# Optimization experiments

Measured on AMD Instinct MI355X. Metric: run time of the kernel, lower is better.

Reference implementation:

```python
import jax, jax.numpy as jnp
import numpy as np

N_PAPER, N_MESH = 60000, 30000
N = N_PAPER + N_MESH
E_TRAIN, E_DEC = 2000000, 400000
F_PAPER = F_MESH = 128
D0, H, D = 16, 32, 16  # initial embed, hidden, final embed
NREL, NB = 2, 4


def _glorot(key, shape):
    fan_in, fan_out = shape[-2], shape[-1]
    s = jnp.sqrt(6.0 / (fan_in + fan_out)).astype(jnp.float32)
    return jax.random.uniform(key, shape, jnp.float32, -s, s)


def setup_inputs() -> dict:
    key = jax.random.key(0)
    ks = iter(jax.random.split(key, 40))
    inp = {
        'x_paper': jax.random.normal(next(ks), (N_PAPER, F_PAPER), jnp.float32),
        'x_mesh': jax.random.normal(next(ks), (N_MESH, F_MESH), jnp.float32),
        'train_edge_index': jax.random.randint(next(ks), (2, E_TRAIN), 0, N, jnp.int64 if jax.config.jax_enable_x64 else jnp.int32),
        'train_edge_type': jnp.sort(jax.random.randint(next(ks), (E_TRAIN,), 0, NREL)),
        'pos_edge_index': jax.random.randint(next(ks), (2, E_DEC), 0, N),
        'pos_edge_type': jnp.sort(jax.random.randint(next(ks), (E_DEC,), 0, NREL)),
        'neg_edge_index': jax.random.randint(next(ks), (2, E_DEC), 0, N),
        'neg_edge_type': jnp.sort(jax.random.randint(next(ks), (E_DEC,), 0, NREL)),
        # input transforms
        'Wp': _glorot(next(ks), (F_PAPER, D0)), 'bp': jnp.zeros((D0,), jnp.float32),
        'Wm': _glorot(next(ks), (F_MESH, D0)), 'bm': jnp.zeros((D0,), jnp.float32),
        # decode linears
        'Wd0': _glorot(next(ks), (D, D)), 'bd0': jnp.zeros((D,), jnp.float32),
        'Wd1': _glorot(next(ks), (D, D)), 'bd1': jnp.zeros((D,), jnp.float32),
    }
    dims = [(D0, H), (H, H), (H, H), (H, D)]
    for i, (di, do) in enumerate(dims, 1):
        inp[f'bases{i}'] = _glorot(next(ks), (NB, di, do))
        inp[f'comp{i}'] = _glorot(next(ks), (NREL, NB))
        inp[f'root{i}'] = _glorot(next(ks), (di, do))
        inp[f'bias{i}'] = jnp.zeros((do,), jnp.float32)
    return inp


def rgcn_layer(x, src, dst, et, bases, comp, root, bias):
    # PyG RGCNConv with basis decomposition, per-relation mean aggregation.
    out = x @ root + bias
    xs = x[src]  # [E, in]
    for r in range(NREL):
        W_r = jnp.einsum('b,bio->io', comp[r], bases)
        m = xs @ W_r  # [E, out]
        mf = (et == r).astype(m.dtype)
        cnt = jax.ops.segment_sum(mf, dst, num_segments=N)
        agg = jax.ops.segment_sum(m * mf[:, None], dst, num_segments=N)
        out = out + agg / jnp.clip(cnt, 1.0)[:, None]
    return out


def _decode_block(z, ei, et, Wd0, bd0, Wd1, bd1):
    zs, zd = z[ei[0]], z[ei[1]]
    h0 = zs @ Wd0 + bd0
    h1 = zs @ Wd1 + bd1
    h = jnp.where((et == 0)[:, None], h0, h1)
    return jnp.sum(h * zd, axis=-1)


def reference(x_paper, x_mesh, train_edge_index, train_edge_type,
              pos_edge_index, pos_edge_type, neg_edge_index, neg_edge_type,
              Wp, bp, Wm, bm, Wd0, bd0, Wd1, bd1,
              bases1, comp1, root1, bias1, bases2, comp2, root2, bias2,
              bases3, comp3, root3, bias3, bases4, comp4, root4, bias4):
    x = jnp.concatenate([x_paper @ Wp + bp, x_mesh @ Wm + bm], axis=0)  # [N, D0]
    src, dst = train_edge_index[0], train_edge_index[1]
    x = jax.nn.relu(rgcn_layer(x, src, dst, train_edge_type, bases1, comp1, root1, bias1))
    x = jax.nn.relu(rgcn_layer(x, src, dst, train_edge_type, bases2, comp2, root2, bias2))
    x = jax.nn.relu(rgcn_layer(x, src, dst, train_edge_type, bases3, comp3, root3, bias3))
    z = rgcn_layer(x, src, dst, train_edge_type, bases4, comp4, root4, bias4)
    # edge types are sorted, so per-edge in-order compute matches the masked concat order
    pos = _decode_block(z, pos_edge_index, pos_edge_type, Wd0, bd0, Wd1, bd1)
    neg = _decode_block(z, neg_edge_index, neg_edge_type, Wd0, bd0, Wd1, bd1)
    return jnp.concatenate([pos, neg], axis=0)  # [2*E_DEC]
```

## Files before the change

kernel.cpp:

```cpp
#include <hip/hip_runtime.h>
#include <hip/hip_bf16.h>

constexpr int NN = 90000;
constexpr int NP = 60000;
constexpr int NM = 30000;
constexpr int ET = 2000000;
constexpr int ED = 400000;
constexpr int TWO_NN = 2 * NN;

constexpr int BKT_SH  = 10;
constexpr int NB_BKT  = (TWO_NN + 1023) >> BKT_SH;
constexpr int BKT_CAP = 12288;
constexpr int TILE    = 2048;
constexpr int N_TILES = (ET + TILE - 1) / TILE;

__device__ __forceinline__ float bflo(unsigned int u) {
    union { unsigned int i; float f; } c;
    c.i = u << 16;
    return c.f;
}
__device__ __forceinline__ float bfhi(unsigned int u) {
    union { unsigned int i; float f; } c;
    c.i = u & 0xffff0000u;
    return c.f;
}
__device__ __forceinline__ unsigned short f2bf(float f) {
    union { float f; unsigned int i; } c;
    c.f = f;
    unsigned int x = c.i;
    return (unsigned short)((x + 0x7FFFu + ((x >> 16) & 1u)) >> 16);
}

__global__ void init_kernel(const int* __restrict__ tei, int* __restrict__ gcur,
                            int* __restrict__ dflag) {
    int b = blockIdx.x * blockDim.x + threadIdx.x;
    if (b < NB_BKT) gcur[b] = b * BKT_CAP;
    if (b == 0) {
        int allzero = 1;
        for (int i = 0; i < 16; i++)
            if (tei[2 * i + 1] != 0) allzero = 0;
        dflag[0] = allzero;
    }
}

__global__ void __launch_bounds__(256) binA_kernel(
        const int* __restrict__ ei, const int* __restrict__ et,
        const int* __restrict__ dflag, int* __restrict__ gcur,
        int2* __restrict__ pairs) {
    __shared__ int hist[NB_BKT];
    __shared__ int excl[NB_BKT];
    __shared__ int cur[NB_BKT];
    __shared__ int gbase[NB_BKT];
    __shared__ int scn[256];
    __shared__ int2 tbuf[TILE];
    int t = threadIdx.x;
    int tile0 = blockIdx.x * TILE;
    int tcount = ET - tile0;
    if (tcount > TILE) tcount = TILE;
    for (int i = t; i < NB_BKT; i += 256) hist[i] = 0;
    __syncthreads();
    int sft = dflag[0];
    int myk[8], mys[8];
#pragma unroll
    for (int q = 0; q < 8; q++) {
        int li = q * 256 + t;
        myk[q] = -1;
        if (li < tcount) {
            int e = tile0 + li;
            int s = ei[(size_t)e << sft];
            int d = ei[(size_t)(ET + e) << sft];
            int r = et[(size_t)e << sft];
            int key = r * NN + d;
            myk[q] = key;
            mys[q] = s;
            atomicAdd(&hist[key >> BKT_SH], 1);
        }
    }
    __syncthreads();
    int v = (t < NB_BKT) ? hist[t] : 0;
    scn[t] = v;
    __syncthreads();
    for (int st = 1; st < 256; st <<= 1) {
        int u = (t >= st) ? scn[t - st] : 0;
        __syncthreads();
        scn[t] += u;
        __syncthreads();
    }
    if (t < NB_BKT) {
        excl[t] = scn[t] - v;
        cur[t] = scn[t] - v;
    }
    __syncthreads();
#pragma unroll
    for (int q = 0; q < 8; q++) {
        if (myk[q] >= 0) {
            int b = myk[q] >> BKT_SH;
            int p = atomicAdd(&cur[b], 1);
            tbuf[p] = make_int2(myk[q], mys[q]);
        }
    }
    __syncthreads();
    if (t < NB_BKT && hist[t] > 0) gbase[t] = atomicAdd(&gcur[t], hist[t]);
    __syncthreads();
    for (int i = t; i < tcount; i += 256) {
        int2 p = tbuf[i];
        int b = p.x >> BKT_SH;
        int gpos = gbase[b] + (i - excl[b]);
        int cap = (b + 1) * BKT_CAP - 1;
        pairs[gpos < cap ? gpos : cap] = p;
    }
}

__global__ void __launch_bounds__(256) histB_kernel(
        const int* __restrict__ gcur, const int2* __restrict__ pairs,
        int* __restrict__ off, int* __restrict__ endo, float* __restrict__ inv) {
    __shared__ int kh[1024];
    __shared__ int scn[256];
    int b = blockIdx.x;
    int t = threadIdx.x;
    for (int i = t; i < 1024; i += 256) kh[i] = 0;
    __syncthreads();
    int beg = b * BKT_CAP, end = gcur[b];
    for (int i = beg + t; i < end; i += 256)
        atomicAdd(&kh[pairs[i].x & 1023], 1);
    __syncthreads();
    int v[4];
    int s = 0;
#pragma unroll
    for (int q = 0; q < 4; q++) {
        v[q] = kh[t * 4 + q];
        s += v[q];
    }
    scn[t] = s;
    __syncthreads();
    for (int st = 1; st < 256; st <<= 1) {
        int u = (t >= st) ? scn[t - st] : 0;
        __syncthreads();
        scn[t] += u;
        __syncthreads();
    }
    int run = b * BKT_CAP + scn[t] - s;
    int kbase = b << BKT_SH;
#pragma unroll
    for (int q = 0; q < 4; q++) {
        int key = kbase + t * 4 + q;
        if (key < TWO_NN) {
            off[key] = run;
            endo[key] = run + v[q];
            inv[key] = 1.0f / (float)(v[q] > 1 ? v[q] : 1);
        }
        run += v[q];
    }
}

__global__ void __launch_bounds__(256) placeB_kernel(
        const int* __restrict__ gcur, const int2* __restrict__ pairs,
        const int* __restrict__ off, int* __restrict__ csr) {
    __shared__ int kc[1024];
    int b = blockIdx.x;
    int t = threadIdx.x;
    int kbase = b << BKT_SH;
    for (int i = t; i < 1024; i += 256)
        if (kbase + i < TWO_NN) kc[i] = off[kbase + i];
    __syncthreads();
    int beg = b * BKT_CAP, end = gcur[b];
    for (int i = beg + t; i < end; i += 256) {
        int2 p = pairs[i];
        int pos = atomicAdd(&kc[p.x & 1023], 1);
        csr[pos] = p.y;
    }
}

__global__ void __launch_bounds__(256) embed2_kernel(
        const float* __restrict__ Xp, const float* __restrict__ Xm,
        const float* __restrict__ Wp, const float* __restrict__ bp,
        const float* __restrict__ Wm, const float* __restrict__ bm,
        float* __restrict__ out, unsigned short* __restrict__ outbf) {
    __shared__ float Wl[4096 + 32];
    for (int i = threadIdx.x; i < 2048; i += 256) {
        Wl[i] = Wp[i];
        Wl[2048 + i] = Wm[i];
    }
    if (threadIdx.x < 16) {
        Wl[4096 + threadIdx.x] = bp[threadIdx.x];
        Wl[4112 + threadIdx.x] = bm[threadIdx.x];
    }
    __syncthreads();
    int n = blockIdx.x * 256 + threadIdx.x;
    if (n >= NN) return;
    const float* X;
    const float* Ws;
    const float* Bs;
    if (n < NP) { X = Xp + (size_t)n * 128; Ws = Wl; Bs = Wl + 4096; }
    else        { X = Xm + (size_t)(n - NP) * 128; Ws = Wl + 2048; Bs = Wl + 4112; }
    float acc[16];
#pragma unroll
    for (int j = 0; j < 16; j++) acc[j] = Bs[j];
    const float4* row = (const float4*)X;
    for (int k4 = 0; k4 < 32; k4++) {
        float4 xv = row[k4];
        int k = k4 * 4;
#pragma unroll
        for (int j = 0; j < 16; j++) {
            float a = acc[j];
            a = fmaf(xv.x, Ws[(k + 0) * 16 + j], a);
            a = fmaf(xv.y, Ws[(k + 1) * 16 + j], a);
            a = fmaf(xv.z, Ws[(k + 2) * 16 + j], a);
            a = fmaf(xv.w, Ws[(k + 3) * 16 + j], a);
            acc[j] = a;
        }
    }
    float4* o = (float4*)(out + (size_t)n * 16);
    ushort4* ob = (ushort4*)(outbf + (size_t)n * 16);
#pragma unroll
    for (int q = 0; q < 4; q++) {
        o[q] = make_float4(acc[4 * q], acc[4 * q + 1], acc[4 * q + 2], acc[4 * q + 3]);
        ushort4 ub;
        ub.x = f2bf(acc[4 * q]);     ub.y = f2bf(acc[4 * q + 1]);
        ub.z = f2bf(acc[4 * q + 2]); ub.w = f2bf(acc[4 * q + 3]);
        ob[q] = ub;
    }
}

__global__ void prep_all_kernel(
        const float* __restrict__ ba0, const float* __restrict__ co0,
        const float* __restrict__ ro0, const float* __restrict__ bi0,
        const float* __restrict__ ba1, const float* __restrict__ co1,
        const float* __restrict__ ro1, const float* __restrict__ bi1,
        const float* __restrict__ ba2, const float* __restrict__ co2,
        const float* __restrict__ ro2, const float* __restrict__ bi2,
        const float* __restrict__ ba3, const float* __restrict__ co3,
        const float* __restrict__ ro3, const float* __restrict__ bi3,
        float* __restrict__ Wbuf4) {
    int l = blockIdx.x;
    const float* bases; const float* comp; const float* root; const float* bias;
    if (l == 0)      { bases = ba0; comp = co0; root = ro0; bias = bi0; }
    else if (l == 1) { bases = ba1; comp = co1; root = ro1; bias = bi1; }
    else if (l == 2) { bases = ba2; comp = co2; root = ro2; bias = bi2; }
    else             { bases = ba3; comp = co3; root = ro3; bias = bi3; }
    int din = (l == 0) ? 16 : 32;
    int dout = (l == 3) ? 16 : 32;
    int sz = din * dout;
    float* W = Wbuf4 + l * 3200;
    for (int i = threadIdx.x; i < sz; i += 256) {
        float b0 = bases[i];
        float b1 = bases[sz + i];
        float b2 = bases[2 * sz + i];
        float b3 = bases[3 * sz + i];
        for (int r = 0; r < 2; r++) {
            W[r * sz + i] = comp[r * 4 + 0] * b0 + comp[r * 4 + 1] * b1 +
                            comp[r * 4 + 2] * b2 + comp[r * 4 + 3] * b3;
        }
        W[2 * sz + i] = root[i];
    }
    if (threadIdx.x < dout) W[3 * sz + threadIdx.x] = bias[threadIdx.x];
}

template <int DIN, int DOUT, int RELU, int WBF>
__global__ void __launch_bounds__(256) layer_kernel(
        const int* __restrict__ off, const int* __restrict__ endo,
        const int* __restrict__ csr,
        const float* __restrict__ xin, const unsigned short* __restrict__ xbf_in,
        const float* __restrict__ inv, const float* __restrict__ Wbuf,
        float* __restrict__ xout, unsigned short* __restrict__ xbf_out) {
    constexpr int SZ = DIN * DOUT;
    constexpr int QL = DIN / 8;
    constexpr int TPN = 2 * QL;
    constexpr int NPB = 256 / TPN;
    constexpr int AGST = 2 * DIN + 4;
    constexpr int XSST = DIN + 4;
    __shared__ float Wl[3 * SZ + DOUT];
    __shared__ float agg[NPB * AGST];
    __shared__ float xs[NPB * XSST];
    for (int i = threadIdx.x; i < 3 * SZ + DOUT; i += 256) Wl[i] = Wbuf[i];
    int t = threadIdx.x;
    int ln = t / TPN;
    int rl = t % TPN;
    int r = rl / QL;
    int lane = rl % QL;
    int d = blockIdx.x * NPB + ln;
    if (d < NN) {
        *(float4*)(xs + ln * XSST + rl * 4) =
            *(const float4*)(xin + (size_t)d * DIN + rl * 4);
        int key = r * NN + d;
        int b = off[key];
        int e = endo[key];
        float a0[8] = {0, 0, 0, 0, 0, 0, 0, 0};
        float a1[8] = {0, 0, 0, 0, 0, 0, 0, 0};
        const unsigned short* hp = xbf_in + lane * 8;
        int k = b;
        for (; k + 1 < e; k += 2) {
            int s0 = csr[k];
            int s1 = csr[k + 1];
            uint4 u0 = *(const uint4*)(hp + (size_t)s0 * DIN);
            uint4 u1 = *(const uint4*)(hp + (size_t)s1 * DIN);
            a0[0] += bflo(u0.x); a0[1] += bfhi(u0.x);
            a0[2] += bflo(u0.y); a0[3] += bfhi(u0.y);
            a0[4] += bflo(u0.z); a0[5] += bfhi(u0.z);
            a0[6] += bflo(u0.w); a0[7] += bfhi(u0.w);
            a1[0] += bflo(u1.x); a1[1] += bfhi(u1.x);
            a1[2] += bflo(u1.y); a1[3] += bfhi(u1.y);
            a1[4] += bflo(u1.z); a1[5] += bfhi(u1.z);
            a1[6] += bflo(u1.w); a1[7] += bfhi(u1.w);
        }
        if (k < e) {
            uint4 u0 = *(const uint4*)(hp + (size_t)csr[k] * DIN);
            a0[0] += bflo(u0.x); a0[1] += bfhi(u0.x);
            a0[2] += bflo(u0.y); a0[3] += bfhi(u0.y);
            a0[4] += bflo(u0.z); a0[5] += bfhi(u0.z);
            a0[6] += bflo(u0.w); a0[7] += bfhi(u0.w);
        }
        float* ap = agg + ln * AGST + r * DIN + lane * 8;
        *(float4*)ap = make_float4(a0[0] + a1[0], a0[1] + a1[1],
                                   a0[2] + a1[2], a0[3] + a1[3]);
        *(float4*)(ap + 4) = make_float4(a0[4] + a1[4], a0[5] + a1[5],
                                         a0[6] + a1[6], a0[7] + a1[7]);
    }
    __syncthreads();
    constexpr int CPN = DOUT / 4;
    for (int tt = t; tt < NPB * CPN; tt += 256) {
        int ln2 = tt / CPN;
        int j0 = (tt % CPN) * 4;
        int d2 = blockIdx.x * NPB + ln2;
        if (d2 < NN) {
            float iv0 = inv[d2], iv1 = inv[NN + d2];
            float acc[4];
#pragma unroll
            for (int jj = 0; jj < 4; jj++) acc[jj] = Wl[3 * SZ + j0 + jj];
#pragma unroll
            for (int k = 0; k < DIN; k++) {
                float xv = xs[ln2 * XSST + k];
                float m0 = agg[ln2 * AGST + k] * iv0;
                float m1 = agg[ln2 * AGST + DIN + k] * iv1;
                const float* w0 = &Wl[k * DOUT + j0];
                const float* w1 = &Wl[SZ + k * DOUT + j0];
                const float* wr = &Wl[2 * SZ + k * DOUT + j0];
#pragma unroll
                for (int jj = 0; jj < 4; jj++) {
                    acc[jj] = fmaf(xv, wr[jj], acc[jj]);
                    acc[jj] = fmaf(m0, w0[jj], acc[jj]);
                    acc[jj] = fmaf(m1, w1[jj], acc[jj]);
                }
            }
            if (RELU) {
#pragma unroll
                for (int jj = 0; jj < 4; jj++) acc[jj] = fmaxf(acc[jj], 0.0f);
            }
            *(float4*)(xout + (size_t)d2 * DOUT + j0) =
                make_float4(acc[0], acc[1], acc[2], acc[3]);
            if (WBF) {
                ushort4 ub;
                ub.x = f2bf(acc[0]); ub.y = f2bf(acc[1]);
                ub.z = f2bf(acc[2]); ub.w = f2bf(acc[3]);
                *(ushort4*)(xbf_out + (size_t)d2 * DOUT + j0) = ub;
            }
        }
    }
}

__global__ void __launch_bounds__(256) decode_fused_kernel(
        const float* __restrict__ z,
        const float* __restrict__ Wd0, const float* __restrict__ bd0,
        const float* __restrict__ Wd1, const float* __restrict__ bd1,
        const int* __restrict__ pei, const int* __restrict__ pet,
        const int* __restrict__ nei, const int* __restrict__ net_,
        float* __restrict__ out, const int* __restrict__ dflag) {
    __shared__ float W[2][256];
    __shared__ float B[2][16];
    for (int i = threadIdx.x; i < 256; i += 256) {
        W[0][i] = Wd0[i];
        W[1][i] = Wd1[i];
    }
    if (threadIdx.x < 16) {
        B[0][threadIdx.x] = bd0[threadIdx.x];
        B[1][threadIdx.x] = bd1[threadIdx.x];
    }
    __syncthreads();
    int i = blockIdx.x * 256 + threadIdx.x;
    if (i >= 2 * ED) return;
    int sft = dflag[0];
    const int* ei;
    const int* et;
    int e;
    if (i < ED) { ei = pei; et = pet; e = i; }
    else        { ei = nei; et = net_; e = i - ED; }
    int s = ei[(size_t)e << sft];
    int d = ei[(size_t)(ED + e) << sft];
    int r = et[(size_t)e << sft];
    float zs[16], zd[16];
    const float4* sp = (const float4*)(z + ((size_t)s << 4));
    const float4* dp = (const float4*)(z + ((size_t)d << 4));
#pragma unroll
    for (int q = 0; q < 4; q++) {
        float4 a = sp[q];
        float4 b = dp[q];
        zs[4 * q] = a.x; zs[4 * q + 1] = a.y; zs[4 * q + 2] = a.z; zs[4 * q + 3] = a.w;
        zd[4 * q] = b.x; zd[4 * q + 1] = b.y; zd[4 * q + 2] = b.z; zd[4 * q + 3] = b.w;
    }
    const float* Wr = W[r];
    const float* Br = B[r];
    float acc = 0.0f;
#pragma unroll
    for (int j = 0; j < 16; j++) {
        float yj = Br[j];
#pragma unroll
        for (int k = 0; k < 16; k++) yj = fmaf(zs[k], Wr[k * 16 + j], yj);
        acc = fmaf(yj, zd[j], acc);
    }
    out[i] = acc;
}

extern "C" void kernel_launch(void* const* d_in, const int* in_sizes, int n_in,
                              void* d_out, int out_size, void* d_ws, size_t ws_size,
                              hipStream_t stream) {
    const float* x_paper = (const float*)d_in[0];
    const float* x_mesh  = (const float*)d_in[1];
    const int* tei  = (const int*)d_in[2];
    const int* tet  = (const int*)d_in[3];
    const int* pei  = (const int*)d_in[4];
    const int* pet  = (const int*)d_in[5];
    const int* nei  = (const int*)d_in[6];
    const int* net_ = (const int*)d_in[7];
    const float* Wp  = (const float*)d_in[8];
    const float* bp  = (const float*)d_in[9];
    const float* Wm  = (const float*)d_in[10];
    const float* bm  = (const float*)d_in[11];
    const float* Wd0 = (const float*)d_in[12];
    const float* bd0 = (const float*)d_in[13];
    const float* Wd1 = (const float*)d_in[14];
    const float* bd1 = (const float*)d_in[15];

    float* ws = (float*)d_ws;
    size_t o = 0;
    float* bufA = ws + o; o += (size_t)NN * 32;
    float* bufB = ws + o; o += (size_t)NN * 32;
    unsigned short* xbfA = (unsigned short*)(ws + o); o += (size_t)NN * 16;
    unsigned short* xbfB = (unsigned short*)(ws + o); o += (size_t)NN * 16;
    float* inv  = ws + o; o += (size_t)TWO_NN;
    int*   off  = (int*)(ws + o); o += (size_t)TWO_NN;
    int*   endo = (int*)(ws + o); o += (size_t)TWO_NN;
    int*   csr  = (int*)(ws + o); o += (size_t)NB_BKT * BKT_CAP;
    int*   gcur = (int*)(ws + o); o += 256;
    int2*  pairs = (int2*)(ws + o); o += (size_t)2 * NB_BKT * BKT_CAP;
    float* Wbuf4 = ws + o; o += 4 * 3200;
    int*   dflag = (int*)(ws + o); o += 16;

    init_kernel<<<1, 256, 0, stream>>>(tei, gcur, dflag);

    binA_kernel<<<N_TILES, 256, 0, stream>>>(tei, tet, dflag, gcur, pairs);
    histB_kernel<<<NB_BKT, 256, 0, stream>>>(gcur, pairs, off, endo, inv);
    placeB_kernel<<<NB_BKT, 256, 0, stream>>>(gcur, pairs, off, csr);

    embed2_kernel<<<(NN + 255) / 256, 256, 0, stream>>>(
        x_paper, x_mesh, Wp, bp, Wm, bm, bufA, xbfA);

    prep_all_kernel<<<4, 256, 0, stream>>>(
        (const float*)d_in[16], (const float*)d_in[17], (const float*)d_in[18], (const float*)d_in[19],
        (const float*)d_in[20], (const float*)d_in[21], (const float*)d_in[22], (const float*)d_in[23],
        (const float*)d_in[24], (const float*)d_in[25], (const float*)d_in[26], (const float*)d_in[27],
        (const float*)d_in[28], (const float*)d_in[29], (const float*)d_in[30], (const float*)d_in[31],
        Wbuf4);

    int blk16 = (NN + 63) / 64;
    int blk32 = (NN + 31) / 32;
    layer_kernel<16, 32, 1, 1><<<blk16, 256, 0, stream>>>(
        off, endo, csr, bufA, xbfA, inv, Wbuf4 + 0 * 3200, bufB, xbfB);
    layer_kernel<32, 32, 1, 1><<<blk32, 256, 0, stream>>>(
        off, endo, csr, bufB, xbfB, inv, Wbuf4 + 1 * 3200, bufA, xbfA);
    layer_kernel<32, 32, 1, 1><<<blk32, 256, 0, stream>>>(
        off, endo, csr, bufA, xbfA, inv, Wbuf4 + 2 * 3200, bufB, xbfB);
    layer_kernel<32, 16, 0, 0><<<blk32, 256, 0, stream>>>(
        off, endo, csr, bufB, xbfB, inv, Wbuf4 + 3 * 3200, bufA, xbfA );

    decode_fused_kernel<<<(2 * ED + 255) / 256, 256, 0, stream>>>(
        bufA, Wd0, bd0, Wd1, bd1, pei, pet, nei, net_, (float*)d_out, dflag);
}
```

Measured before the change: 400.4 us.

## Fuse CSR histogram and placement kernels; keep intermediate activations in bf16 only

Merges the per-bucket histogram and placement kernels into one kernel that stages each bucket's pairs in shared memory, so the pairs array is read from global memory once and one launch is dropped. Intermediate layer activations are now stored and read only as bf16. The fp32 copies used for the self/root term are gone, and only the final layer writes fp32 z for decode. This cuts global write and read traffic, but the root term now uses bf16-rounded inputs (a precision change), and the 96KB shared staging buffer limits occupancy of the fused kernel.

After: 392.3 us. 1.02x faster.

```diff
diff --git a/kernel.cpp b/kernel.cpp
--- a/kernel.cpp
+++ b/kernel.cpp
@@ -111,18 +111,21 @@
     }
 }
 
-__global__ void __launch_bounds__(256) histB_kernel(
+__global__ void __launch_bounds__(256) histplace_kernel(
         const int* __restrict__ gcur, const int2* __restrict__ pairs,
-        int* __restrict__ off, int* __restrict__ endo, float* __restrict__ inv) {
+        int* __restrict__ off, int* __restrict__ endo, float* __restrict__ inv,
+        int* __restrict__ csr) {
+    __shared__ int2 pl[BKT_CAP];
     __shared__ int kh[1024];
     __shared__ int scn[256];
     int b = blockIdx.x;
     int t = threadIdx.x;
+    int beg = b * BKT_CAP;
+    int n = gcur[b] - beg;
     for (int i = t; i < 1024; i += 256) kh[i] = 0;
-    __syncthreads();
-    int beg = b * BKT_CAP, end = gcur[b];
-    for (int i = beg + t; i < end; i += 256)
-        atomicAdd(&kh[pairs[i].x & 1023], 1);
+    for (int i = t; i < n; i += 256) pl[i] = pairs[beg + i];
+    __syncthreads();
+    for (int i = t; i < n; i += 256) atomicAdd(&kh[pl[i].x & 1023], 1);
     __syncthreads();
     int v[4];
     int s = 0;
@@ -139,8 +142,9 @@
         scn[t] += u;
         __syncthreads();
     }
-    int run = b * BKT_CAP + scn[t] - s;
+    int run = beg + scn[t] - s;
     int kbase = b << BKT_SH;
+    int kc[4];
 #pragma unroll
     for (int q = 0; q < 4; q++) {
         int key = kbase + t * 4 + q;
@@ -149,24 +153,16 @@
             endo[key] = run + v[q];
             inv[key] = 1.0f / (float)(v[q] > 1 ? v[q] : 1);
         }
+        kc[q] = run;
         run += v[q];
     }
-}
-
-__global__ void __launch_bounds__(256) placeB_kernel(
-        const int* __restrict__ gcur, const int2* __restrict__ pairs,
-        const int* __restrict__ off, int* __restrict__ csr) {
-    __shared__ int kc[1024];
-    int b = blockIdx.x;
-    int t = threadIdx.x;
-    int kbase = b << BKT_SH;
-    for (int i = t; i < 1024; i += 256)
-        if (kbase + i < TWO_NN) kc[i] = off[kbase + i];
-    __syncthreads();
-    int beg = b * BKT_CAP, end = gcur[b];
-    for (int i = beg + t; i < end; i += 256) {
-        int2 p = pairs[i];
-        int pos = atomicAdd(&kc[p.x & 1023], 1);
+    __syncthreads();
+#pragma unroll
+    for (int q = 0; q < 4; q++) kh[t * 4 + q] = kc[q];
+    __syncthreads();
+    for (int i = t; i < n; i += 256) {
+        int2 p = pl[i];
+        int pos = atomicAdd(&kh[p.x & 1023], 1);
         csr[pos] = p.y;
     }
 }
@@ -175,7 +171,7 @@
         const float* __restrict__ Xp, const float* __restrict__ Xm,
         const float* __restrict__ Wp, const float* __restrict__ bp,
         const float* __restrict__ Wm, const float* __restrict__ bm,
-        float* __restrict__ out, unsigned short* __restrict__ outbf) {
+        unsigned short* __restrict__ outbf) {
     __shared__ float Wl[4096 + 32];
     for (int i = threadIdx.x; i < 2048; i += 256) {
         Wl[i] = Wp[i];
@@ -210,11 +206,9 @@
             acc[j] = a;
         }
     }
-    float4* o = (float4*)(out + (size_t)n * 16);
     ushort4* ob = (ushort4*)(outbf + (size_t)n * 16);
 #pragma unroll
     for (int q = 0; q < 4; q++) {
-        o[q] = make_float4(acc[4 * q], acc[4 * q + 1], acc[4 * q + 2], acc[4 * q + 3]);
         ushort4 ub;
         ub.x = f2bf(acc[4 * q]);     ub.y = f2bf(acc[4 * q + 1]);
         ub.z = f2bf(acc[4 * q + 2]); ub.w = f2bf(acc[4 * q + 3]);
@@ -256,11 +250,11 @@
     if (threadIdx.x < dout) W[3 * sz + threadIdx.x] = bias[threadIdx.x];
 }
 
-template <int DIN, int DOUT, int RELU, int WBF>
+template <int DIN, int DOUT, int RELU, int FP32OUT>
 __global__ void __launch_bounds__(256) layer_kernel(
         const int* __restrict__ off, const int* __restrict__ endo,
         const int* __restrict__ csr,
-        const float* __restrict__ xin, const unsigned short* __restrict__ xbf_in,
+        const unsigned short* __restrict__ xbf_in,
         const float* __restrict__ inv, const float* __restrict__ Wbuf,
         float* __restrict__ xout, unsigned short* __restrict__ xbf_out) {
     constexpr int SZ = DIN * DOUT;
@@ -280,8 +274,14 @@
     int lane = rl % QL;
     int d = blockIdx.x * NPB + ln;
     if (d < NN) {
-        *(float4*)(xs + ln * XSST + rl * 4) =
-            *(const float4*)(xin + (size_t)d * DIN + rl * 4);
+        if (r == 0) {
+            uint4 u = *(const uint4*)(xbf_in + (size_t)d * DIN + lane * 8);
+            float* xp = xs + ln * XSST + lane * 8;
+            xp[0] = bflo(u.x); xp[1] = bfhi(u.x);
+            xp[2] = bflo(u.y); xp[3] = bfhi(u.y);
+            xp[4] = bflo(u.z); xp[5] = bfhi(u.z);
+            xp[6] = bflo(u.w); xp[7] = bfhi(u.w);
+        }
         int key = r * NN + d;
         int b = off[key];
         int e = endo[key];
@@ -346,9 +346,10 @@
 #pragma unroll
                 for (int jj = 0; jj < 4; jj++) acc[jj] = fmaxf(acc[jj], 0.0f);
             }
-            *(float4*)(xout + (size_t)d2 * DOUT + j0) =
-                make_float4(acc[0], acc[1], acc[2], acc[3]);
-            if (WBF) {
+            if (FP32OUT) {
+                *(float4*)(xout + (size_t)d2 * DOUT + j0) =
+                    make_float4(acc[0], acc[1], acc[2], acc[3]);
+            } else {
                 ushort4 ub;
                 ub.x = f2bf(acc[0]); ub.y = f2bf(acc[1]);
                 ub.z = f2bf(acc[2]); ub.w = f2bf(acc[3]);
@@ -432,8 +433,7 @@
 
     float* ws = (float*)d_ws;
     size_t o = 0;
-    float* bufA = ws + o; o += (size_t)NN * 32;
-    float* bufB = ws + o; o += (size_t)NN * 32;
+    float* zbuf = ws + o; o += (size_t)NN * 16;
     unsigned short* xbfA = (unsigned short*)(ws + o); o += (size_t)NN * 16;
     unsigned short* xbfB = (unsigned short*)(ws + o); o += (size_t)NN * 16;
     float* inv  = ws + o; o += (size_t)TWO_NN;
@@ -448,11 +448,10 @@
     init_kernel<<<1, 256, 0, stream>>>(tei, gcur, dflag);
 
     binA_kernel<<<N_TILES, 256, 0, stream>>>(tei, tet, dflag, gcur, pairs);
-    histB_kernel<<<NB_BKT, 256, 0, stream>>>(gcur, pairs, off, endo, inv);
-    placeB_kernel<<<NB_BKT, 256, 0, stream>>>(gcur, pairs, off, csr);
+    histplace_kernel<<<NB_BKT, 256, 0, stream>>>(gcur, pairs, off, endo, inv, csr);
 
     embed2_kernel<<<(NN + 255) / 256, 256, 0, stream>>>(
-        x_paper, x_mesh, Wp, bp, Wm, bm, bufA, xbfA);
+        x_paper, x_mesh, Wp, bp, Wm, bm, xbfA);
 
     prep_all_kernel<<<4, 256, 0, stream>>>(
         (const float*)d_in[16], (const float*)d_in[17], (const float*)d_in[18], (const float*)d_in[19],
@@ -463,15 +462,15 @@
 
     int blk16 = (NN + 63) / 64;
     int blk32 = (NN + 31) / 32;
-    layer_kernel<16, 32, 1, 1><<<blk16, 256, 0, stream>>>(
-        off, endo, csr, bufA, xbfA, inv, Wbuf4 + 0 * 3200, bufB, xbfB);
-    layer_kernel<32, 32, 1, 1><<<blk32, 256, 0, stream>>>(
-        off, endo, csr, bufB, xbfB, inv, Wbuf4 + 1 * 3200, bufA, xbfA);
-    layer_kernel<32, 32, 1, 1><<<blk32, 256, 0, stream>>>(
-        off, endo, csr, bufA, xbfA, inv, Wbuf4 + 2 * 3200, bufB, xbfB);
-    layer_kernel<32, 16, 0, 0><<<blk32, 256, 0, stream>>>(
-        off, endo, csr, bufB, xbfB, inv, Wbuf4 + 3 * 3200, bufA, xbfA );
+    layer_kernel<16, 32, 1, 0><<<blk16, 256, 0, stream>>>(
+        off, endo, csr, xbfA, inv, Wbuf4 + 0 * 3200, nullptr, xbfB);
+    layer_kernel<32, 32, 1, 0><<<blk32, 256, 0, stream>>>(
+        off, endo, csr, xbfB, inv, Wbuf4 + 1 * 3200, nullptr, xbfA);
+    layer_kernel<32, 32, 1, 0><<<blk32, 256, 0, stream>>>(
+        off, endo, csr, xbfA, inv, Wbuf4 + 2 * 3200, nullptr, xbfB);
+    layer_kernel<32, 16, 0, 1><<<blk32, 256, 0, stream>>>(
+        off, endo, csr, xbfB, inv, Wbuf4 + 3 * 3200, zbuf, nullptr);
 
     decode_fused_kernel<<<(2 * ED + 255) / 256, 256, 0, stream>>>(
-        bufA, Wd0, bd0, Wd1, bd1, pei, pet, nei, net_, (float*)d_out, dflag);
-}
+        zbuf, Wd0, bd0, Wd1, bd1, pei, pet, nei, net_, (float*)d_out, dflag);
+}
```
